# Kernel tuning notes

Measured on AMD Instinct MI355X. Metric: run time of the kernel, lower is better.

## Reference

```python
import jax, jax.numpy as jnp
import numpy as np

WAY, SHOT, QUERY = 64, 8, 16


def setup_inputs() -> dict:
    key = jax.random.key(0)
    k1, k2 = jax.random.split(key)
    t, c = 32, 1024
    query_feat = jax.random.normal(k1, (t, WAY * QUERY, c), dtype=jnp.float32)
    support_feat = jax.random.normal(k2, (t, WAY * SHOT, c), dtype=jnp.float32)
    return {"query_feat": query_feat, "support_feat": support_feat}


def reference(query_feat, support_feat):
    t, wq, c = query_feat.shape
    # prototypes: mean over shots -> [t, way, c]
    proto = jnp.mean(support_feat.reshape(t, WAY, SHOT, c), axis=2)
    # squared Euclidean via expansion: ||q||^2 - 2 q.p + ||p||^2
    q_sq = jnp.sum(query_feat * query_feat, axis=-1, keepdims=True)      # [t, wq, 1]
    p_sq = jnp.sum(proto * proto, axis=-1)[:, None, :]                   # [t, 1, way]
    qp = jnp.einsum('tqc,twc->tqw', query_feat, proto)                   # [t, wq, way]
    dist = -(q_sq - 2.0 * qp + p_sq)
    return dist
```

## Files before the change

### kernel.cpp

```cpp
#include <hip/hip_runtime.h>
#include <hip/hip_bf16.h>

#define T 32
#define WAYS 64
#define SHOTS 8
#define CDIM 1024
#define WQ 1024
#define NK 16

typedef float f32x4 __attribute__((ext_vector_type(4)));
typedef __bf16 bf16x8 __attribute__((ext_vector_type(8)));

__global__ __launch_bounds__(256) void proto_kernel(const float* __restrict__ support,
                                                    __bf16* __restrict__ proto,
                                                    float* __restrict__ p_sq) {
    const int bid = blockIdx.x;
    const int tid = threadIdx.x;
    const float* sp = support + (size_t)bid * (SHOTS * CDIM);
    float4 a = make_float4(0.f, 0.f, 0.f, 0.f);
#pragma unroll
    for (int s = 0; s < SHOTS; ++s) {
        const float4 v = *reinterpret_cast<const float4*>(sp + s * CDIM + tid * 4);
        a.x += v.x; a.y += v.y; a.z += v.z; a.w += v.w;
    }
    a.x *= 0.125f; a.y *= 0.125f; a.z *= 0.125f; a.w *= 0.125f;
    float ps = a.x * a.x + a.y * a.y + a.z * a.z + a.w * a.w;

    union { __bf16 h[4]; uint2 u; } pk;
    pk.h[0] = (__bf16)a.x; pk.h[1] = (__bf16)a.y; pk.h[2] = (__bf16)a.z; pk.h[3] = (__bf16)a.w;
    *reinterpret_cast<uint2*>(proto + (size_t)bid * CDIM + tid * 4) = pk.u;

#pragma unroll
    for (int m = 32; m >= 1; m >>= 1) ps += __shfl_down(ps, m, 64);
    __shared__ float red[4];
    const int wv = tid >> 6, ln = tid & 63;
    if (ln == 0) red[wv] = ps;
    __syncthreads();
    if (tid == 0) p_sq[bid] = red[0] + red[1] + red[2] + red[3];
}

__global__ __launch_bounds__(512, 4) void dist_kernel(const float* __restrict__ query,
                                                      const __bf16* __restrict__ proto,
                                                      const float* __restrict__ p_sq,
                                                      float* __restrict__ out) {
    const int bx  = blockIdx.x;
    const int t   = bx >> 4;
    const int mt  = bx & 15;
    const int tid = threadIdx.x;
    const int lane = tid & 63;
    const int wid  = tid >> 6;
    const int wr   = wid >> 1;
    const int wn   = wid & 1;
    const int fr   = lane & 15;
    const int kg   = lane >> 4;

    __shared__ __bf16 As[2][64 * 64];
    __shared__ __bf16 Bs[2][64 * 64];
    __shared__ float qsq_s[64];

    const int srow = tid >> 3;
    const int sk8  = tid & 7;

    const float*  qbase = query + ((size_t)(t * WQ + mt * 64 + srow)) * CDIM;
    const __bf16* pbase = proto + ((size_t)(t * WAYS + srow)) * CDIM;

    struct Stage { f32x4 a0, a1; uint4 b; };

    auto LOAD = [&](int ks) -> Stage {
        Stage s;
        s.a0 = *reinterpret_cast<const f32x4*>(qbase + ks * 64 + sk8 * 4);
        s.a1 = *reinterpret_cast<const f32x4*>(qbase + ks * 64 + 32 + sk8 * 4);
        s.b  = *reinterpret_cast<const uint4*>(pbase + ks * 64 + sk8 * 8);
        return s;
    };

    float qsq = 0.f;

    auto WRITE = [&](int buf, const Stage& s) {
        qsq += s.a0.x * s.a0.x + s.a0.y * s.a0.y + s.a0.z * s.a0.z + s.a0.w * s.a0.w +
               s.a1.x * s.a1.x + s.a1.y * s.a1.y + s.a1.z * s.a1.z + s.a1.w * s.a1.w;
        union { __bf16 h[4]; uint2 u; } p0, p1;
        p0.h[0] = (__bf16)s.a0.x; p0.h[1] = (__bf16)s.a0.y;
        p0.h[2] = (__bf16)s.a0.z; p0.h[3] = (__bf16)s.a0.w;
        p1.h[0] = (__bf16)s.a1.x; p1.h[1] = (__bf16)s.a1.y;
        p1.h[2] = (__bf16)s.a1.z; p1.h[3] = (__bf16)s.a1.w;
        char* ab = reinterpret_cast<char*>(As[buf]);
        const int swz = (srow & 7) << 4;
        *reinterpret_cast<uint2*>(ab + ((srow * 128 + sk8 * 8) ^ swz))      = p0.u;
        *reinterpret_cast<uint2*>(ab + ((srow * 128 + 64 + sk8 * 8) ^ swz)) = p1.u;
        char* bb = reinterpret_cast<char*>(Bs[buf]);
        *reinterpret_cast<uint4*>(bb + ((srow * 128 + sk8 * 16) ^ swz))     = s.b;
    };

    f32x4 acc[2];
    acc[0] = (f32x4){0.f, 0.f, 0.f, 0.f};
    acc[1] = (f32x4){0.f, 0.f, 0.f, 0.f};

    auto COMPUTE = [&](int buf) {
        const char* ab = reinterpret_cast<const char*>(As[buf]);
        const char* bb = reinterpret_cast<const char*>(Bs[buf]);
#pragma unroll
        for (int ksub = 0; ksub < 2; ++ksub) {
            const int arow = wr * 16 + fr;
            const bf16x8 af = *reinterpret_cast<const bf16x8*>(
                ab + ((arow * 128 + ksub * 64 + kg * 16) ^ ((arow & 7) << 4)));
#pragma unroll
            for (int nf = 0; nf < 2; ++nf) {
                const int way = wn * 32 + nf * 16 + fr;
                const bf16x8 bf = *reinterpret_cast<const bf16x8*>(
                    bb + ((way * 128 + ksub * 64 + kg * 16) ^ ((way & 7) << 4)));
                acc[nf] = __builtin_amdgcn_mfma_f32_16x16x32_bf16(af, bf, acc[nf], 0, 0, 0);
            }
        }
    };

    Stage s0 = LOAD(0);
    Stage sA = LOAD(1);
    Stage sB = LOAD(2);
    WRITE(0, s0);
    asm volatile("s_waitcnt lgkmcnt(0)" ::: "memory");
    __builtin_amdgcn_s_barrier();

#pragma unroll
    for (int ks = 0; ks < NK; ++ks) {
        Stage nx;
        if (ks < NK - 3) nx = LOAD(ks + 3);
        COMPUTE(ks & 1);
        if (ks < NK - 1) WRITE((ks + 1) & 1, sA);
        sA = sB; sB = nx;
        asm volatile("s_waitcnt lgkmcnt(0)" ::: "memory");
        __builtin_amdgcn_s_barrier();
    }

    qsq += __shfl_xor(qsq, 1, 64);
    qsq += __shfl_xor(qsq, 2, 64);
    qsq += __shfl_xor(qsq, 4, 64);
    if (sk8 == 0) qsq_s[srow] = qsq;
    __syncthreads();

    float psqv[2];
#pragma unroll
    for (int nf = 0; nf < 2; ++nf)
        psqv[nf] = p_sq[t * WAYS + wn * 32 + nf * 16 + fr];

    float* ob = out + ((size_t)(t * WQ + mt * 64 + wr * 16)) * WAYS;
#pragma unroll
    for (int r = 0; r < 4; ++r) {
        const int row = kg * 4 + r;
        const float qv = qsq_s[wr * 16 + row];
#pragma unroll
        for (int nf = 0; nf < 2; ++nf) {
            ob[(size_t)row * WAYS + wn * 32 + nf * 16 + fr] =
                2.f * acc[nf][r] - qv - psqv[nf];
        }
    }
}

extern "C" void kernel_launch(void* const* d_in, const int* in_sizes, int n_in,
                              void* d_out, int out_size, void* d_ws, size_t ws_size,
                              hipStream_t stream) {
    const float* query   = (const float*)d_in[0];
    const float* support = (const float*)d_in[1];
    float* out = (float*)d_out;

    __bf16* proto = (__bf16*)d_ws;
    float*  p_sq  = (float*)((char*)d_ws + (size_t)T * WAYS * CDIM * sizeof(__bf16));

    hipLaunchKernelGGL(proto_kernel, dim3(T * WAYS), dim3(256), 0, stream,
                       support, proto, p_sq);
    hipLaunchKernelGGL(dist_kernel, dim3(T * 16), dim3(512), 0, stream,
                       query, proto, p_sq, out);
}
```

Baseline: 41.66 us.

## Double K-tile depth to 128, remap blocks across XCDs, hoist p_sq load

```diff
diff --git a/kernel.cpp b/kernel.cpp
--- a/kernel.cpp
+++ b/kernel.cpp
@@ -6,7 +6,8 @@
 #define SHOTS 8
 #define CDIM 1024
 #define WQ 1024
-#define NK 16
+#define BK 128
+#define NK 8
 
 typedef float f32x4 __attribute__((ext_vector_type(4)));
 typedef __bf16 bf16x8 __attribute__((ext_vector_type(8)));
@@ -43,9 +44,10 @@
                                                       const __bf16* __restrict__ proto,
                                                       const float* __restrict__ p_sq,
                                                       float* __restrict__ out) {
-    const int bx  = blockIdx.x;
-    const int t   = bx >> 4;
-    const int mt  = bx & 15;
+    const int bx = blockIdx.x;
+    const int vb = (bx & 7) * 64 + (bx >> 3);
+    const int t   = vb >> 4;
+    const int mt  = vb & 15;
     const int tid = threadIdx.x;
     const int lane = tid & 63;
     const int wid  = tid >> 6;
@@ -54,42 +56,52 @@
     const int fr   = lane & 15;
     const int kg   = lane >> 4;
 
-    __shared__ __bf16 As[2][64 * 64];
-    __shared__ __bf16 Bs[2][64 * 64];
+    __shared__ __bf16 As[2][64 * BK];
+    __shared__ __bf16 Bs[2][64 * BK];
     __shared__ float qsq_s[64];
 
     const int srow = tid >> 3;
     const int sk8  = tid & 7;
 
-    const float*  qbase = query + ((size_t)(t * WQ + mt * 64 + srow)) * CDIM;
-    const __bf16* pbase = proto + ((size_t)(t * WAYS + srow)) * CDIM;
+    const float*  qbase = query + ((size_t)(t * WQ + mt * 64 + srow)) * CDIM + sk8 * 16;
+    const __bf16* pbase = proto + ((size_t)(t * WAYS + srow)) * CDIM + sk8 * 16;
 
-    struct Stage { f32x4 a0, a1; uint4 b; };
+    struct Stage { f32x4 a[4]; uint4 b[2]; };
 
     auto LOAD = [&](int ks) -> Stage {
         Stage s;
-        s.a0 = *reinterpret_cast<const f32x4*>(qbase + ks * 64 + sk8 * 4);
-        s.a1 = *reinterpret_cast<const f32x4*>(qbase + ks * 64 + 32 + sk8 * 4);
-        s.b  = *reinterpret_cast<const uint4*>(pbase + ks * 64 + sk8 * 8);
+        const float* ap = qbase + ks * BK;
+#pragma unroll
+        for (int p = 0; p < 4; ++p)
+            s.a[p] = *reinterpret_cast<const f32x4*>(ap + p * 4);
+        const __bf16* bp = pbase + ks * BK;
+        s.b[0] = *reinterpret_cast<const uint4*>(bp);
+        s.b[1] = *reinterpret_cast<const uint4*>(bp + 8);
         return s;
     };
 
     float qsq = 0.f;
 
     auto WRITE = [&](int buf, const Stage& s) {
-        qsq += s.a0.x * s.a0.x + s.a0.y * s.a0.y + s.a0.z * s.a0.z + s.a0.w * s.a0.w +
-               s.a1.x * s.a1.x + s.a1.y * s.a1.y + s.a1.z * s.a1.z + s.a1.w * s.a1.w;
-        union { __bf16 h[4]; uint2 u; } p0, p1;
-        p0.h[0] = (__bf16)s.a0.x; p0.h[1] = (__bf16)s.a0.y;
-        p0.h[2] = (__bf16)s.a0.z; p0.h[3] = (__bf16)s.a0.w;
-        p1.h[0] = (__bf16)s.a1.x; p1.h[1] = (__bf16)s.a1.y;
-        p1.h[2] = (__bf16)s.a1.z; p1.h[3] = (__bf16)s.a1.w;
+#pragma unroll
+        for (int p = 0; p < 4; ++p)
+            qsq += s.a[p].x * s.a[p].x + s.a[p].y * s.a[p].y +
+                   s.a[p].z * s.a[p].z + s.a[p].w * s.a[p].w;
+        union { __bf16 h[8]; uint4 u; } p0, p1;
+#pragma unroll
+        for (int j = 0; j < 2; ++j) {
+            const f32x4 v0 = s.a[j * 2], v1 = s.a[j * 2 + 1];
+            __bf16* h = (j == 0) ? p0.h : p1.h;
+            h[0] = (__bf16)v0.x; h[1] = (__bf16)v0.y; h[2] = (__bf16)v0.z; h[3] = (__bf16)v0.w;
+            h[4] = (__bf16)v1.x; h[5] = (__bf16)v1.y; h[6] = (__bf16)v1.z; h[7] = (__bf16)v1.w;
+        }
+        const int swz = (srow & 7) << 4;
         char* ab = reinterpret_cast<char*>(As[buf]);
-        const int swz = (srow & 7) << 4;
-        *reinterpret_cast<uint2*>(ab + ((srow * 128 + sk8 * 8) ^ swz))      = p0.u;
-        *reinterpret_cast<uint2*>(ab + ((srow * 128 + 64 + sk8 * 8) ^ swz)) = p1.u;
+        *reinterpret_cast<uint4*>(ab + ((srow * 256 + sk8 * 32) ^ swz))      = p0.u;
+        *reinterpret_cast<uint4*>(ab + ((srow * 256 + sk8 * 32 + 16) ^ swz)) = p1.u;
         char* bb = reinterpret_cast<char*>(Bs[buf]);
-        *reinterpret_cast<uint4*>(bb + ((srow * 128 + sk8 * 16) ^ swz))     = s.b;
+        *reinterpret_cast<uint4*>(bb + ((srow * 256 + sk8 * 32) ^ swz))      = s.b[0];
+        *reinterpret_cast<uint4*>(bb + ((srow * 256 + sk8 * 32 + 16) ^ swz)) = s.b[1];
     };
 
     f32x4 acc[2];
@@ -100,23 +112,27 @@
         const char* ab = reinterpret_cast<const char*>(As[buf]);
         const char* bb = reinterpret_cast<const char*>(Bs[buf]);
 #pragma unroll
-        for (int ksub = 0; ksub < 2; ++ksub) {
+        for (int ksub = 0; ksub < 4; ++ksub) {
             const int arow = wr * 16 + fr;
             const bf16x8 af = *reinterpret_cast<const bf16x8*>(
-                ab + ((arow * 128 + ksub * 64 + kg * 16) ^ ((arow & 7) << 4)));
+                ab + ((arow * 256 + ksub * 64 + kg * 16) ^ ((arow & 7) << 4)));
 #pragma unroll
             for (int nf = 0; nf < 2; ++nf) {
                 const int way = wn * 32 + nf * 16 + fr;
                 const bf16x8 bf = *reinterpret_cast<const bf16x8*>(
-                    bb + ((way * 128 + ksub * 64 + kg * 16) ^ ((way & 7) << 4)));
+                    bb + ((way * 256 + ksub * 64 + kg * 16) ^ ((way & 7) << 4)));
                 acc[nf] = __builtin_amdgcn_mfma_f32_16x16x32_bf16(af, bf, acc[nf], 0, 0, 0);
             }
         }
     };
 
+    float psqv[2];
+#pragma unroll
+    for (int nf = 0; nf < 2; ++nf)
+        psqv[nf] = p_sq[t * WAYS + wn * 32 + nf * 16 + fr];
+
     Stage s0 = LOAD(0);
     Stage sA = LOAD(1);
-    Stage sB = LOAD(2);
     WRITE(0, s0);
     asm volatile("s_waitcnt lgkmcnt(0)" ::: "memory");
     __builtin_amdgcn_s_barrier();
@@ -124,10 +140,10 @@
 #pragma unroll
     for (int ks = 0; ks < NK; ++ks) {
         Stage nx;
-        if (ks < NK - 3) nx = LOAD(ks + 3);
+        if (ks < NK - 2) nx = LOAD(ks + 2);
         COMPUTE(ks & 1);
         if (ks < NK - 1) WRITE((ks + 1) & 1, sA);
-        sA = sB; sB = nx;
+        sA = nx;
         asm volatile("s_waitcnt lgkmcnt(0)" ::: "memory");
         __builtin_amdgcn_s_barrier();
     }
@@ -137,11 +153,6 @@
     qsq += __shfl_xor(qsq, 4, 64);
     if (sk8 == 0) qsq_s[srow] = qsq;
     __syncthreads();
-
-    float psqv[2];
-#pragma unroll
-    for (int nf = 0; nf < 2; ++nf)
-        psqv[nf] = p_sq[t * WAYS + wn * 32 + nf * 16 + fr];
 
     float* ob = out + ((size_t)(t * WQ + mt * 64 + wr * 16)) * WAYS;
 #pragma unroll
```

Result: faster. 38.87 us (-6.7%).
